# Optimization experiments

Hardware: AMD Instinct MI355X
Metric: run time of the kernel (lower is better)

## Reference

```python
import jax, jax.numpy as jnp
import numpy as np

N = 100000      # total nodes
E = 800000      # directed edges
DIN = 256       # input feature dim
H = 128         # hidden dim
EPS = 1e-5      # BatchNorm eps


def setup_inputs() -> dict:
    key = jax.random.key(0)
    ks = jax.random.split(key, 18)
    s = 0.05
    return {
        "x": jax.random.normal(ks[0], (N, DIN), jnp.float32),
        "src": jax.random.randint(ks[1], (E,), 0, N, dtype=jnp.int32),
        "dst": jax.random.randint(ks[2], (E,), 0, N, dtype=jnp.int32),
        "W1": jax.random.normal(ks[3], (DIN, H), jnp.float32) * s,
        "b1": jnp.zeros((H,), jnp.float32),
        "g1": jnp.ones((H,), jnp.float32),
        "be1": jnp.zeros((H,), jnp.float32),
        "W2": jax.random.normal(ks[4], (H, H), jnp.float32) * s,
        "b2": jnp.zeros((H,), jnp.float32),
        "g2": jnp.ones((H,), jnp.float32),
        "be2": jnp.zeros((H,), jnp.float32),
        "W3": jax.random.normal(ks[5], (H, H), jnp.float32) * s,
        "b3": jnp.zeros((H,), jnp.float32),
        "g3": jnp.ones((H,), jnp.float32),
        "be3": jnp.zeros((H,), jnp.float32),
        "Wf": jax.random.normal(ks[6], (H, 1), jnp.float32) * s,
        "bf": jnp.zeros((1,), jnp.float32),
    }


def _gcn_conv(h, W, b, src, dst, dis):
    # GCNConv: project, then sym-normalized aggregation over edges + self-loops
    h = h @ W                                   # [N, out]
    coef = dis[src] * dis[dst]                  # [E] edge norm weights
    agg = jax.ops.segment_sum(h[src] * coef[:, None], dst, num_segments=N)
    agg = agg + h * (dis * dis)[:, None]        # self-loop term (norm = 1/deg)
    return agg + b


def _bn_relu(h, g, be):
    # BatchNorm1d in training mode (batch stats over nodes, biased variance)
    mu = jnp.mean(h, axis=0)
    var = jnp.var(h, axis=0)
    return jax.nn.relu((h - mu) * (g / jnp.sqrt(var + EPS)) + be)


def reference(x, src, dst, W1, b1, g1, be1, W2, b2, g2, be2,
              W3, b3, g3, be3, Wf, bf):
    # degree of (A + I) counted on destination nodes, edge weight 1
    deg = jax.ops.segment_sum(jnp.ones((E,), jnp.float32), dst, num_segments=N) + 1.0
    dis = jax.lax.rsqrt(deg)                    # deg >= 1, safe

    h = _bn_relu(_gcn_conv(x, W1, b1, src, dst, dis), g1, be1)
    h = _bn_relu(_gcn_conv(h, W2, b2, src, dst, dis), g2, be2)
    h = _bn_relu(_gcn_conv(h, W3, b3, src, dst, dis), g3, be3)
    return h @ Wf + bf                          # [N, 1]
```

## Files before the change

### kernel.cpp

```cpp
#include <hip/hip_runtime.h>
#include <hip/hip_bf16.h>

typedef unsigned short ushort_t;
typedef __bf16 bf16x8 __attribute__((ext_vector_type(8)));
typedef unsigned short ushort8 __attribute__((ext_vector_type(8)));
typedef unsigned short ushort4v __attribute__((ext_vector_type(4)));
typedef float f32x4 __attribute__((ext_vector_type(4)));

#define HH 128
#define EPS 1e-5f
#define STAT_SLICES 32
#define GAS __attribute__((address_space(1)))
#define LAS __attribute__((address_space(3)))

__device__ __forceinline__ float bf2f(ushort_t u) {
    unsigned v = ((unsigned)u) << 16;
    return __builtin_bit_cast(float, v);
}
__device__ __forceinline__ ushort_t f2bf(float f) {
    unsigned u = __builtin_bit_cast(unsigned, f);
    unsigned r = (u + 0x7fffu + ((u >> 16) & 1u)) >> 16;
    return (ushort_t)r;
}
__device__ __forceinline__ float cvt(const void* p, int i, int flag) {
    return flag ? bf2f(((const ushort_t*)p)[i]) : ((const float*)p)[i];
}
__device__ __forceinline__ void dma16(const void* g, void* l) {
    __builtin_amdgcn_global_load_lds((const GAS unsigned*)g, (LAS unsigned*)l, 16, 0, 0);
}
__device__ __forceinline__ void acc8(const uint4 w, float c, float a[8]) {
    unsigned x0 = w.x, x1 = w.y, x2 = w.z, x3 = w.w;
    a[0] = fmaf(__builtin_bit_cast(float, x0 << 16), c, a[0]);
    a[1] = fmaf(__builtin_bit_cast(float, x0 & 0xffff0000u), c, a[1]);
    a[2] = fmaf(__builtin_bit_cast(float, x1 << 16), c, a[2]);
    a[3] = fmaf(__builtin_bit_cast(float, x1 & 0xffff0000u), c, a[3]);
    a[4] = fmaf(__builtin_bit_cast(float, x2 << 16), c, a[4]);
    a[5] = fmaf(__builtin_bit_cast(float, x2 & 0xffff0000u), c, a[5]);
    a[6] = fmaf(__builtin_bit_cast(float, x3 << 16), c, a[6]);
    a[7] = fmaf(__builtin_bit_cast(float, x3 & 0xffff0000u), c, a[7]);
}

__global__ void preK(const int* __restrict__ dst, int* __restrict__ counts, int E,
                     const void* W1, ushort_t* Wt1, const void* W2, ushort_t* Wt2,
                     const void* W3, ushort_t* Wt3,
                     const void* g1, const void* b1, const void* b2, const void* b3,
                     const void* g2, const void* g3, const void* be1, const void* be2,
                     const void* be3, const void* Wfp, const void* bfp,
                     float* __restrict__ cvec, int histB) {
    const int bid = blockIdx.x;
    const int tid = threadIdx.x;
    const int flag = (((const ushort_t*)g1)[0] == 0x3F80) ? 1 : 0;
    if (bid < histB) {
        int e = bid * 256 + tid;
        if (e < E) atomicAdd(&counts[dst[e]], 1);
    } else if (bid < histB + 256) {
        int idx = (bid - histB) * 256 + tid;
        const void* W; ushort_t* Wt; int K;
        if (idx < 32768)      { W = W1; Wt = Wt1; K = 256; }
        else if (idx < 49152) { W = W2; Wt = Wt2; K = 128; idx -= 32768; }
        else                  { W = W3; Wt = Wt3; K = 128; idx -= 49152; }
        int k = idx >> 7, nn = idx & 127;
        Wt[nn * K + k] = flag ? ((const ushort_t*)W)[idx] : f2bf(((const float*)W)[idx]);
    } else {
        int t = tid;
        if (t < 128) {
            cvec[t]        = cvt(b1, t, flag);
            cvec[128 + t]  = cvt(b2, t, flag);
            cvec[256 + t]  = cvt(b3, t, flag);
            cvec[384 + t]  = cvt(g1, t, flag);
            cvec[512 + t]  = cvt(g2, t, flag);
            cvec[640 + t]  = cvt(g3, t, flag);
            cvec[768 + t]  = cvt(be1, t, flag);
            cvec[896 + t]  = cvt(be2, t, flag);
            cvec[1024 + t] = cvt(be3, t, flag);
            cvec[1152 + t] = cvt(Wfp, t, flag);
            if (t == 0) cvec[1280] = cvt(bfp, 0, flag);
        }
    }
}

__global__ void scanAdisK(const int* __restrict__ cnt, int* __restrict__ partial,
                          float* __restrict__ dis, int n, int nbScan) {
    __shared__ int lds[256];
    const int tid = threadIdx.x;
    if ((int)blockIdx.x < nbScan) {
        int base = blockIdx.x * 2048 + tid * 8;
        int s = 0;
#pragma unroll
        for (int j = 0; j < 8; ++j) { int idx = base + j; if (idx < n) s += cnt[idx]; }
        lds[tid] = s; __syncthreads();
        for (int off = 128; off; off >>= 1) { if (tid < off) lds[tid] += lds[tid + off]; __syncthreads(); }
        if (tid == 0) partial[blockIdx.x] = lds[0];
    } else {
        int i = (blockIdx.x - nbScan) * 256 + tid;
        if (i < n) dis[i] = rsqrtf((float)cnt[i] + 1.0f);
    }
}

__device__ __forceinline__ void scanC2Dev(int* lds, const int* __restrict__ cnt,
                                          const int* __restrict__ partial,
                                          int* __restrict__ rowptr, int n, int bid, int nb) {
    const int tid = threadIdx.x;
    int pre = 0, tot = 0;
    for (int i = 0; i < nb; ++i) { int v = partial[i]; if (i < bid) pre += v; tot += v; }
    int base = bid * 2048 + tid * 8;
    int v[8]; int s = 0;
#pragma unroll
    for (int j = 0; j < 8; ++j) { int idx = base + j; v[j] = (idx < n) ? cnt[idx] : 0; s += v[j]; }
    lds[tid] = s; __syncthreads();
    for (int off = 1; off < 256; off <<= 1) {
        int x = (tid >= off) ? lds[tid - off] : 0;
        __syncthreads();
        lds[tid] += x;
        __syncthreads();
    }
    int excl = lds[tid] - s;
    int off0 = pre + excl;
#pragma unroll
    for (int j = 0; j < 8; ++j) {
        int idx = base + j;
        if (idx < n) { rowptr[idx] = off0; off0 += v[j]; }
    }
    if (bid == 0 && tid == 0) rowptr[n] = tot;
}

__global__ void scatterK(const int* __restrict__ src, const int* __restrict__ dst,
                         const int* __restrict__ rowptr, int* __restrict__ fill,
                         const float* __restrict__ dis,
                         uint2* __restrict__ erec, int E) {
    int e = blockIdx.x * 256 + threadIdx.x;
    if (e >= E) return;
    int d = dst[e], s = src[e];
    int old = atomicSub(&fill[d], 1);
    int pos = rowptr[d] + old - 1;
    float c = dis[s] * dis[d];
    uint2 r; r.x = (unsigned)s; r.y = __builtin_bit_cast(unsigned, c);
    erec[pos] = r;
}

__global__ __launch_bounds__(256) void mm1scanCK(const void* __restrict__ x,
                                                 const ushort_t* __restrict__ Wt1,
                                                 ushort_t* __restrict__ tbuf, int n,
                                                 const ushort_t* __restrict__ flagRef,
                                                 const int* __restrict__ cnt,
                                                 const int* __restrict__ partial,
                                                 int* __restrict__ rowptr, int nbScan) {
    __shared__ char smem[65536];
    const int tid = threadIdx.x;
    if ((int)blockIdx.x < nbScan) {
        scanC2Dev((int*)smem, cnt, partial, rowptr, n, blockIdx.x, nbScan);
        return;
    }
    const int arm = blockIdx.x - nbScan;

#pragma unroll
    for (int it = 0; it < 16; ++it) {
        int idx = tid + it * 256;
        int r = idx >> 5, seg = idx & 31;
        int p = seg ^ (r & 7);
        *(uint4*)&smem[r * 512 + p * 16] = *(const uint4*)&Wt1[(size_t)r * 256 + seg * 8];
    }
    __syncthreads();

    const int lane = tid & 63, wave = tid >> 6;
    const int m = lane & 15, q = lane >> 4;
    const int flag = (flagRef[0] == 0x3F80) ? 1 : 0;
    const int nTiles = (n + 63) >> 6;

    auto loadA = [&](int tile, ushort8 af[8]) {
        int node = tile * 64 + wave * 16 + m;
        int rr = node < n ? node : n - 1;
        if (flag) {
            const ushort_t* ap = (const ushort_t*)x + (size_t)rr * 256 + q * 8;
#pragma unroll
            for (int s = 0; s < 8; ++s) af[s] = *(const ushort8*)(ap + s * 32);
        } else {
            const float* ap = (const float*)x + (size_t)rr * 256 + q * 8;
#pragma unroll
            for (int s = 0; s < 8; ++s) {
                float4 f0 = *(const float4*)(ap + s * 32);
                float4 f1 = *(const float4*)(ap + s * 32 + 4);
                ushort8 v;
                v[0] = f2bf(f0.x); v[1] = f2bf(f0.y); v[2] = f2bf(f0.z); v[3] = f2bf(f0.w);
                v[4] = f2bf(f1.x); v[5] = f2bf(f1.y); v[6] = f2bf(f1.z); v[7] = f2bf(f1.w);
                af[s] = v;
            }
        }
    };

    ushort8 afA[8];
    if (arm < nTiles) loadA(arm, afA);

    for (int tile = arm; tile < nTiles; tile += 512) {
        ushort8 afB[8];
        int nx = tile + 512;
        if (nx < nTiles) loadA(nx, afB);

        f32x4 acc[8];
#pragma unroll
        for (int t = 0; t < 8; ++t) acc[t] = (f32x4){0.f, 0.f, 0.f, 0.f};
#pragma unroll
        for (int s = 0; s < 8; ++s) {
            bf16x8 nf = __builtin_bit_cast(bf16x8, afA[s]);
            int p = (s * 4 + q) ^ (m & 7);
#pragma unroll
            for (int t = 0; t < 8; ++t) {
                ushort8 wv = *(const ushort8*)&smem[(t * 16 + m) * 512 + p * 16];
                acc[t] = __builtin_amdgcn_mfma_f32_16x16x32_bf16(
                    __builtin_bit_cast(bf16x8, wv), nf, acc[t], 0, 0, 0);
            }
        }
        int node = tile * 64 + wave * 16 + m;
        if (node < n) {
            ushort_t* op = tbuf + (size_t)node * HH + q * 4;
#pragma unroll
            for (int t = 0; t < 8; ++t) {
                ushort4v pk;
#pragma unroll
                for (int r = 0; r < 4; ++r) pk[r] = f2bf(acc[t][r]);
                *(ushort4v*)(op + t * 16) = pk;
            }
        }
#pragma unroll
        for (int s = 0; s < 8; ++s) afA[s] = afB[s];
    }
}

__global__ __launch_bounds__(256) void mmBNK(const ushort_t* __restrict__ A,
                                             const ushort_t* __restrict__ Wt,
                                             ushort_t* __restrict__ out, int n,
                                             const float* __restrict__ ssum,
                                             const float* __restrict__ ssq,
                                             const float* __restrict__ gam,
                                             const float* __restrict__ bet) {
    __shared__ char smem[50176];
    char* abuf = smem + 32768;
    float* scw = (float*)(smem + 49152);
    const int tid = threadIdx.x;

    if (tid < 128) {
        float S = 0.f, Q = 0.f;
#pragma unroll
        for (int sl = 0; sl < STAT_SLICES; ++sl) { S += ssum[sl * HH + tid]; Q += ssq[sl * HH + tid]; }
        float invn = 1.0f / (float)n;
        float mu = S * invn;
        float var = fmaxf(Q * invn - mu * mu, 0.f);
        float sc = gam[tid] * rsqrtf(var + EPS);
        scw[tid] = sc;
        scw[128 + tid] = bet[tid] - mu * sc;
    }
#pragma unroll
    for (int it = 0; it < 8; ++it) {
        int idx = tid + it * 256;
        int r = idx >> 4, seg = idx & 15;
        int p = seg ^ (r & 7);
        *(uint4*)&smem[r * 256 + p * 16] = *(const uint4*)&Wt[(size_t)r * 128 + seg * 8];
    }
    __syncthreads();

    const int lane = tid & 63, wave = tid >> 6;
    const int m = lane & 15, q = lane >> 4;
    const int nTiles = (n + 63) >> 6;

    for (int tile = blockIdx.x; tile < nTiles; tile += gridDim.x) {
        const int row0 = tile * 64 + wave * 16;
#pragma unroll
        for (int j = 0; j < 4; ++j) {
            int r = row0 + j * 4;
            if (r + 3 >= n) r = n - 4;
            const char* g = (const char*)A + (size_t)r * 256 + lane * 16;
            dma16(g, abuf + (wave * 16 + j * 4) * 256);
        }
        __builtin_amdgcn_s_waitcnt(0x0F70);

        f32x4 acc[8];
#pragma unroll
        for (int t = 0; t < 8; ++t) acc[t] = (f32x4){0.f, 0.f, 0.f, 0.f};
        const char* arow = abuf + (wave * 16 + m) * 256;
#pragma unroll
        for (int s = 0; s < 4; ++s) {
            ushort8 av = *(const ushort8*)(arow + s * 64 + q * 16);
            int kb = s * 32 + q * 8;
#pragma unroll
            for (int j = 0; j < 8; ++j)
                av[j] = f2bf(fmaxf(bf2f(av[j]) * scw[kb + j] + scw[128 + kb + j], 0.f));
            bf16x8 nf = __builtin_bit_cast(bf16x8, av);
#pragma unroll
            for (int t = 0; t < 8; ++t) {
                int p = (s * 4 + q) ^ (m & 7);
                ushort8 wv = *(const ushort8*)&smem[(t * 16 + m) * 256 + p * 16];
                acc[t] = __builtin_amdgcn_mfma_f32_16x16x32_bf16(
                    __builtin_bit_cast(bf16x8, wv), nf, acc[t], 0, 0, 0);
            }
        }
        int node = tile * 64 + wave * 16 + m;
        if (node < n) {
            ushort_t* op = out + (size_t)node * HH + q * 4;
#pragma unroll
            for (int t = 0; t < 8; ++t) {
                ushort4v pk;
#pragma unroll
                for (int r = 0; r < 4; ++r) pk[r] = f2bf(acc[t][r]);
                *(ushort4v*)(op + t * 16) = pk;
            }
        }
    }
}

__global__ __launch_bounds__(256) void aggK(const ushort_t* __restrict__ t,
                                            const uint2* __restrict__ erec,
                                            const int* __restrict__ rowptr,
                                            const float* __restrict__ dis,
                                            const float* __restrict__ bias,
                                            ushort_t* __restrict__ g,
                                            float* __restrict__ ssum, float* __restrict__ ssq,
                                            int n) {
    const int tid  = threadIdx.x;
    const int lane = tid & 63;
    const int wave = tid >> 6;
    const int grp  = lane >> 4;
    const int p    = lane & 15;
    const int cb   = p * 8;

    float bch[8];
#pragma unroll
    for (int j = 0; j < 8; ++j) bch[j] = bias[cb + j];

    float s[8], q[8];
#pragma unroll
    for (int j = 0; j < 8; ++j) { s[j] = 0.f; q[j] = 0.f; }

    for (int node = blockIdx.x * 16 + wave * 4 + grp; node < n; node += gridDim.x * 16) {
        float d = dis[node];
        float d2 = d * d;
        float a[8];
#pragma unroll
        for (int j = 0; j < 8; ++j) a[j] = 0.f;
        uint4 sv = *(const uint4*)(t + (size_t)node * HH + cb);
        acc8(sv, d2, a);

        int beg = rowptr[node], end = rowptr[node + 1];
        for (int eb = beg; eb < end; eb += 16) {
            int rem = end - eb; if (rem > 16) rem = 16;
            uint2 rec = (p < rem) ? erec[eb + p] : (uint2){0u, 0u};
            int es = (int)rec.x;
            float ec = __builtin_bit_cast(float, rec.y);
            int rr = (rem + 3) & ~3;
            for (int k = 0; k < rr; k += 4) {
                uint4 ww[4]; float c2[4];
#pragma unroll
                for (int kk = 0; kk < 4; ++kk) {
                    int sl = (lane & 48) + k + kk;
                    int ii = __shfl(es, sl);
                    float cv = __shfl(ec, sl);
                    c2[kk] = (k + kk < rem) ? cv : 0.f;
                    ww[kk] = *(const uint4*)(t + (size_t)ii * HH + cb);
                }
#pragma unroll
                for (int kk = 0; kk < 4; ++kk) acc8(ww[kk], c2[kk], a);
            }
        }
        ushort8 pk;
#pragma unroll
        for (int j = 0; j < 8; ++j) {
            a[j] += bch[j];
            pk[j] = f2bf(a[j]);
            s[j] += a[j]; q[j] += a[j] * a[j];
        }
        *(ushort8*)(g + (size_t)node * HH + cb) = pk;
    }

#pragma unroll
    for (int j = 0; j < 8; ++j) {
        s[j] += __shfl_xor(s[j], 16); s[j] += __shfl_xor(s[j], 32);
        q[j] += __shfl_xor(q[j], 16); q[j] += __shfl_xor(q[j], 32);
    }
    __shared__ float red[4][16][16];
    if (grp == 0) {
#pragma unroll
        for (int j = 0; j < 8; ++j) { red[wave][p][j] = s[j]; red[wave][p][8 + j] = q[j]; }
    }
    __syncthreads();
    {
        int ch = tid & 127, kind = tid >> 7;
        float S = 0.f;
#pragma unroll
        for (int w = 0; w < 4; ++w) S += red[w][ch >> 3][kind * 8 + (ch & 7)];
        int slice = (blockIdx.x & (STAT_SLICES - 1)) * HH;
        atomicAdd((kind ? ssq : ssum) + slice + ch, S);
    }
}

__global__ __launch_bounds__(256) void outK(const ushort_t* __restrict__ g,
                                            const float* __restrict__ ssum,
                                            const float* __restrict__ ssq,
                                            const float* __restrict__ gam,
                                            const float* __restrict__ bet,
                                            const float* __restrict__ Wf,
                                            const float* __restrict__ bfp,
                                            void* __restrict__ outv, int n,
                                            const ushort_t* __restrict__ flagRef) {
    __shared__ float scw[256];
    const int tid = threadIdx.x;
    if (tid < 128) {
        float S = 0.f, Q = 0.f;
#pragma unroll
        for (int sl = 0; sl < STAT_SLICES; ++sl) { S += ssum[sl * HH + tid]; Q += ssq[sl * HH + tid]; }
        float invn = 1.0f / (float)n;
        float mu = S * invn;
        float var = fmaxf(Q * invn - mu * mu, 0.f);
        float sc = gam[tid] * rsqrtf(var + EPS);
        scw[tid] = sc;
        scw[128 + tid] = bet[tid] - mu * sc;
    }
    __syncthreads();

    const int lane = tid & 63;
    const int wave = tid >> 6;
    const int grp  = lane >> 4;
    const int p    = lane & 15;
    const int cb   = p * 8;
    float w8[8], sc8[8], sh8[8];
#pragma unroll
    for (int j = 0; j < 8; ++j) {
        w8[j] = Wf[cb + j]; sc8[j] = scw[cb + j]; sh8[j] = scw[128 + cb + j];
    }
    const float bb = bfp[0];
    const int flag = (flagRef[0] == 0x3F80) ? 1 : 0;

    for (int node = blockIdx.x * 16 + wave * 4 + grp; node < n; node += gridDim.x * 16) {
        uint4 v = *(const uint4*)(g + (size_t)node * HH + cb);
        unsigned u[4] = {v.x, v.y, v.z, v.w};
        float x = 0.f;
#pragma unroll
        for (int j = 0; j < 4; ++j) {
            float f0 = __builtin_bit_cast(float, u[j] << 16);
            float f1 = __builtin_bit_cast(float, u[j] & 0xffff0000u);
            x += fmaxf(f0 * sc8[2 * j] + sh8[2 * j], 0.f) * w8[2 * j];
            x += fmaxf(f1 * sc8[2 * j + 1] + sh8[2 * j + 1], 0.f) * w8[2 * j + 1];
        }
#pragma unroll
        for (int off = 8; off; off >>= 1) x += __shfl_xor(x, off);
        if (p == 0) {
            float r = x + bb;
            if (flag) ((ushort_t*)outv)[node] = f2bf(r);
            else      ((float*)outv)[node] = r;
        }
    }
}

extern "C" void kernel_launch(void* const* d_in, const int* in_sizes, int n_in,
                              void* d_out, int out_size, void* d_ws, size_t ws_size,
                              hipStream_t stream) {
    const int DIN = 256;
    const int N = in_sizes[0] / DIN;
    const int E = in_sizes[1];

    const void* x   = d_in[0];
    const int*  src = (const int*)d_in[1];
    const int*  dst = (const int*)d_in[2];
    const void* W1  = d_in[3];
    const void* b1  = d_in[4];
    const void* g1  = d_in[5];
    const void* be1 = d_in[6];
    const void* W2  = d_in[7];
    const void* b2  = d_in[8];
    const void* g2  = d_in[9];
    const void* be2 = d_in[10];
    const void* W3  = d_in[11];
    const void* b3  = d_in[12];
    const void* g3  = d_in[13];
    const void* be3 = d_in[14];
    const void* Wf  = d_in[15];
    const void* bfp = d_in[16];
    const ushort_t* flagRef = (const ushort_t*)g1;

    char* base = (char*)d_ws;
    size_t off = 0;
    auto carve = [&](size_t bytes) -> void* {
        void* p = base + off;
        off += (bytes + 255) & ~(size_t)255;
        return p;
    };
    int*      counts = (int*)carve((size_t)N * 4);
    float*    stats  = (float*)carve((size_t)3 * 2 * STAT_SLICES * HH * 4);
    size_t    zbytes = off;
    float*    dis    = (float*)carve((size_t)N * 4);
    int*      rowptr = (int*)carve((size_t)(N + 1) * 4);
    int*      partial= (int*)carve(256 * 4);
    uint2*    erec   = (uint2*)carve((size_t)E * 8);
    ushort_t* Wt1    = (ushort_t*)carve((size_t)128 * 256 * 2);
    ushort_t* Wt2    = (ushort_t*)carve((size_t)128 * 128 * 2);
    ushort_t* Wt3    = (ushort_t*)carve((size_t)128 * 128 * 2);
    ushort_t* tbuf   = (ushort_t*)carve((size_t)N * HH * 2);
    ushort_t* gbuf   = (ushort_t*)carve((size_t)N * HH * 2);
    float*    cvec   = (float*)carve((size_t)1281 * 4);

    float* ssum0 = stats;                         float* ssq0 = ssum0 + STAT_SLICES * HH;
    float* ssum1 = ssq0 + STAT_SLICES * HH;       float* ssq1 = ssum1 + STAT_SLICES * HH;
    float* ssum2 = ssq1 + STAT_SLICES * HH;       float* ssq2 = ssum2 + STAT_SLICES * HH;

    float* c_b1 = cvec;         float* c_b2 = cvec + 128;  float* c_b3 = cvec + 256;
    float* c_g1 = cvec + 384;   float* c_g2 = cvec + 512;  float* c_g3 = cvec + 640;
    float* c_be1 = cvec + 768;  float* c_be2 = cvec + 896; float* c_be3 = cvec + 1024;
    float* c_Wf = cvec + 1152;  float* c_bf = cvec + 1280;

    const int nbScan = (N + 2047) / 2048;
    const int histB  = (E + 255) / 256;
    const int disB   = (N + 255) / 256;
    const int aggB   = 2048;

    hipMemsetAsync(d_ws, 0, zbytes, stream);

    preK<<<histB + 256 + 1, 256, 0, stream>>>(dst, counts, E, W1, Wt1, W2, Wt2, W3, Wt3,
                                              g1, b1, b2, b3, g2, g3, be1, be2, be3, Wf, bfp,
                                              cvec, histB);
    scanAdisK<<<nbScan + disB, 256, 0, stream>>>(counts, partial, dis, N, nbScan);
    mm1scanCK<<<nbScan + 512, 256, 0, stream>>>(x, Wt1, tbuf, N, flagRef,
                                                counts, partial, rowptr, nbScan);
    scatterK<<<histB, 256, 0, stream>>>(src, dst, rowptr, counts, dis, erec, E);

    aggK<<<aggB, 256, 0, stream>>>(tbuf, erec, rowptr, dis, c_b1, gbuf, ssum0, ssq0, N);
    mmBNK<<<768, 256, 0, stream>>>(gbuf, Wt2, tbuf, N, ssum0, ssq0, c_g1, c_be1);
    aggK<<<aggB, 256, 0, stream>>>(tbuf, erec, rowptr, dis, c_b2, gbuf, ssum1, ssq1, N);
    mmBNK<<<768, 256, 0, stream>>>(gbuf, Wt3, tbuf, N, ssum1, ssq1, c_g2, c_be2);
    aggK<<<aggB, 256, 0, stream>>>(tbuf, erec, rowptr, dis, c_b3, gbuf, ssum2, ssq2, N);
    outK<<<1024, 256, 0, stream>>>(gbuf, ssum2, ssq2, c_g3, c_be3, c_Wf, c_bf, d_out, N, flagRef);
}
```

Measured before the change: 428.9 us.

## Restructure first-layer GEMM: register-resident W1 fragments, LDS double-buffered X tiles

After: 420.7 us. Within noise of the previous version (-1.9%).

```diff
diff --git a/kernel.cpp b/kernel.cpp
--- a/kernel.cpp
+++ b/kernel.cpp
@@ -10,6 +10,7 @@
 #define HH 128
 #define EPS 1e-5f
 #define STAT_SLICES 32
+#define MTILE 32
 #define GAS __attribute__((address_space(1)))
 #define LAS __attribute__((address_space(3)))
 
@@ -145,84 +146,110 @@
                                                  const int* __restrict__ cnt,
                                                  const int* __restrict__ partial,
                                                  int* __restrict__ rowptr, int nbScan) {
-    __shared__ char smem[65536];
+    __shared__ char smem[33792];
     const int tid = threadIdx.x;
     if ((int)blockIdx.x < nbScan) {
         scanC2Dev((int*)smem, cnt, partial, rowptr, n, blockIdx.x, nbScan);
         return;
     }
     const int arm = blockIdx.x - nbScan;
-
-#pragma unroll
-    for (int it = 0; it < 16; ++it) {
-        int idx = tid + it * 256;
-        int r = idx >> 5, seg = idx & 31;
-        int p = seg ^ (r & 7);
-        *(uint4*)&smem[r * 512 + p * 16] = *(const uint4*)&Wt1[(size_t)r * 256 + seg * 8];
-    }
-    __syncthreads();
+    const int NB  = gridDim.x - nbScan;
+    const int nTiles = (n + MTILE - 1) / MTILE;
+    if (arm >= nTiles) return;
 
     const int lane = tid & 63, wave = tid >> 6;
     const int m = lane & 15, q = lane >> 4;
     const int flag = (flagRef[0] == 0x3F80) ? 1 : 0;
-    const int nTiles = (n + 63) >> 6;
-
-    auto loadA = [&](int tile, ushort8 af[8]) {
-        int node = tile * 64 + wave * 16 + m;
-        int rr = node < n ? node : n - 1;
+
+    ushort8 wfrag[8][2];
+#pragma unroll
+    for (int s = 0; s < 8; ++s)
+#pragma unroll
+        for (int tt = 0; tt < 2; ++tt)
+            wfrag[s][tt] = *(const ushort8*)&Wt1[(size_t)((wave * 2 + tt) * 16 + m) * 256 + s * 32 + q * 8];
+
+    const int sr = tid >> 3, sa = tid & 7;
+    char* buf0 = smem;
+    char* buf1 = smem + 16384;
+
+    float4  f[8];
+    ushort8 v[4];
+
+    auto stageLoad = [&](int T) {
+        int row = T * MTILE + sr; if (row >= n) row = n - 1;
         if (flag) {
-            const ushort_t* ap = (const ushort_t*)x + (size_t)rr * 256 + q * 8;
-#pragma unroll
-            for (int s = 0; s < 8; ++s) af[s] = *(const ushort8*)(ap + s * 32);
+            const ushort_t* xp = (const ushort_t*)x + (size_t)row * 256 + sa * 32;
+#pragma unroll
+            for (int j = 0; j < 4; ++j) v[j] = *(const ushort8*)(xp + j * 8);
         } else {
-            const float* ap = (const float*)x + (size_t)rr * 256 + q * 8;
+            const float* xp = (const float*)x + (size_t)row * 256 + sa * 32;
+#pragma unroll
+            for (int j = 0; j < 8; ++j) f[j] = *(const float4*)(xp + j * 4);
+        }
+    };
+    auto convWrite = [&](char* buf) {
+        if (!flag) {
+#pragma unroll
+            for (int j = 0; j < 4; ++j) {
+                float4 a = f[2 * j], b = f[2 * j + 1];
+                ushort8 t8;
+                t8[0] = f2bf(a.x); t8[1] = f2bf(a.y); t8[2] = f2bf(a.z); t8[3] = f2bf(a.w);
+                t8[4] = f2bf(b.x); t8[5] = f2bf(b.y); t8[6] = f2bf(b.z); t8[7] = f2bf(b.w);
+                v[j] = t8;
+            }
+        }
+#pragma unroll
+        for (int j = 0; j < 4; ++j) {
+            int u = (sa * 4 + j) ^ (sr & 7);
+            *(ushort8*)(buf + sr * 512 + u * 16) = v[j];
+        }
+    };
+    auto computeStore = [&](int T, const char* buf) {
+        f32x4 acc[2][2];
+#pragma unroll
+        for (int bb = 0; bb < 2; ++bb)
+#pragma unroll
+            for (int tt = 0; tt < 2; ++tt) acc[bb][tt] = (f32x4){0.f, 0.f, 0.f, 0.f};
+#pragma unroll
+        for (int bb = 0; bb < 2; ++bb) {
+            const char* base = buf + (bb * 16 + m) * 512;
 #pragma unroll
             for (int s = 0; s < 8; ++s) {
-                float4 f0 = *(const float4*)(ap + s * 32);
-                float4 f1 = *(const float4*)(ap + s * 32 + 4);
-                ushort8 v;
-                v[0] = f2bf(f0.x); v[1] = f2bf(f0.y); v[2] = f2bf(f0.z); v[3] = f2bf(f0.w);
-                v[4] = f2bf(f1.x); v[5] = f2bf(f1.y); v[6] = f2bf(f1.z); v[7] = f2bf(f1.w);
-                af[s] = v;
+                ushort8 xf = *(const ushort8*)(base + (((s * 4 + q) ^ (m & 7)) * 16));
+                bf16x8 xb = __builtin_bit_cast(bf16x8, xf);
+#pragma unroll
+                for (int tt = 0; tt < 2; ++tt)
+                    acc[bb][tt] = __builtin_amdgcn_mfma_f32_16x16x32_bf16(
+                        __builtin_bit_cast(bf16x8, wfrag[s][tt]), xb, acc[bb][tt], 0, 0, 0);
             }
         }
+#pragma unroll
+        for (int bb = 0; bb < 2; ++bb) {
+            int node = T * MTILE + bb * 16 + m;
+            if (node < n) {
+#pragma unroll
+                for (int tt = 0; tt < 2; ++tt) {
+                    ushort4v pk;
+#pragma unroll
+                    for (int r = 0; r < 4; ++r) pk[r] = f2bf(acc[bb][tt][r]);
+                    *(ushort4v*)(tbuf + (size_t)node * HH + (wave * 2 + tt) * 16 + q * 4) = pk;
+                }
+            }
+        }
     };
 
-    ushort8 afA[8];
-    if (arm < nTiles) loadA(arm, afA);
-
-    for (int tile = arm; tile < nTiles; tile += 512) {
-        ushort8 afB[8];
-        int nx = tile + 512;
-        if (nx < nTiles) loadA(nx, afB);
-
-        f32x4 acc[8];
-#pragma unroll
-        for (int t = 0; t < 8; ++t) acc[t] = (f32x4){0.f, 0.f, 0.f, 0.f};
-#pragma unroll
-        for (int s = 0; s < 8; ++s) {
-            bf16x8 nf = __builtin_bit_cast(bf16x8, afA[s]);
-            int p = (s * 4 + q) ^ (m & 7);
-#pragma unroll
-            for (int t = 0; t < 8; ++t) {
-                ushort8 wv = *(const ushort8*)&smem[(t * 16 + m) * 512 + p * 16];
-                acc[t] = __builtin_amdgcn_mfma_f32_16x16x32_bf16(
-                    __builtin_bit_cast(bf16x8, wv), nf, acc[t], 0, 0, 0);
-            }
-        }
-        int node = tile * 64 + wave * 16 + m;
-        if (node < n) {
-            ushort_t* op = tbuf + (size_t)node * HH + q * 4;
-#pragma unroll
-            for (int t = 0; t < 8; ++t) {
-                ushort4v pk;
-#pragma unroll
-                for (int r = 0; r < 4; ++r) pk[r] = f2bf(acc[t][r]);
-                *(ushort4v*)(op + t * 16) = pk;
-            }
-        }
-#pragma unroll
-        for (int s = 0; s < 8; ++s) afA[s] = afB[s];
+    stageLoad(arm); convWrite(buf0);
+    __syncthreads();
+    int T = arm, pp = 0;
+    while (true) {
+        int Tn = T + NB;
+        bool more = (Tn < nTiles);
+        if (more) stageLoad(Tn);
+        computeStore(T, pp ? buf1 : buf0);
+        if (!more) break;
+        convWrite(pp ? buf0 : buf1);
+        __syncthreads();
+        T = Tn; pp ^= 1;
     }
 }
 
@@ -509,6 +536,7 @@
     const int histB  = (E + 255) / 256;
     const int disB   = (N + 255) / 256;
     const int aggB   = 2048;
+    const int mm1B   = 1024;
 
     hipMemsetAsync(d_ws, 0, zbytes, stream);
 
@@ -516,8 +544,8 @@
                                               g1, b1, b2, b3, g2, g3, be1, be2, be3, Wf, bfp,
                                               cvec, histB);
     scanAdisK<<<nbScan + disB, 256, 0, stream>>>(counts, partial, dis, N, nbScan);
-    mm1scanCK<<<nbScan + 512, 256, 0, stream>>>(x, Wt1, tbuf, N, flagRef,
-                                                counts, partial, rowptr, nbScan);
+    mm1scanCK<<<nbScan + mm1B, 256, 0, stream>>>(x, Wt1, tbuf, N, flagRef,
+                                                 counts, partial, rowptr, nbScan);
     scatterK<<<histB, 256, 0, stream>>>(src, dst, rowptr, counts, dis, erec, E);
 
     aggK<<<aggB, 256, 0, stream>>>(tbuf, erec, rowptr, dis, c_b1, gbuf, ssum0, ssq0, N);
```
